# Performance work log

Hardware: AMD Instinct MI355X
Metric: run time of the kernel (lower is better)

Reference implementation:

```python
import jax, jax.numpy as jnp
import numpy as np

NUM_LAYERS = 3  # min_num_layers == max_num_layers == 3 (deterministic stochastic depth)
LN_EPS = 1e-5


def setup_inputs() -> dict:
    key = jax.random.key(0)
    k1, k2, k3 = jax.random.split(key, 3)
    N, d, F = 8, 16, 512  # (batch, in_dim=out_dim, num_features)
    x = jax.random.normal(k1, (N, d, F), dtype=jnp.float32)
    W = jax.random.normal(k2, (d, F, F, d), dtype=jnp.float32)  # recurrent weight
    A = jax.random.uniform(k3, (2, F, F), dtype=jnp.float32)    # transition mats, steps 1..2
    return {"x": x, "W": W, "A": A}


def _contract(h, W, a):
    # h: (N,d,F), W: (d,F,F,o), a: (F,F) -> (N,o,F)
    # Equivalent to (h.unsqueeze(-1).unsqueeze(-1) * (W * a[...,None])).sum(1).sum(1).transpose(1,2)
    return jnp.einsum('ndf,dfgo,fg->nog', h, W, a)


def _layer_norm(y):
    # torch applies layer_norm over the channel dim (axis 1 of (N,o,F)), no affine params
    m = y.mean(axis=1, keepdims=True)
    v = y.var(axis=1, keepdims=True)
    return (y - m) / jnp.sqrt(v + LN_EPS)


def reference(x, W, A):
    history = [x]
    for i in range(1, NUM_LAYERS):
        # recurrent + residual branch: average contributions from all previous layers
        ys = [_contract(history[j], W, A[i - j - 1]) for j in range(i)]
        y = jnp.mean(jnp.stack(ys, axis=0), axis=0)
        y = _layer_norm(y)
        history.append(y)
    return history[-1]  # return_layers='last'
```

## Files before the change

### kernel.cpp

```cpp
#include <hip/hip_runtime.h>
#include <stdint.h>


#define F_CHUNK 32
#define N_CHUNKS 16

__global__ void k0_prep_x(const float* __restrict__ x, float* __restrict__ xT) {
    int idx = blockIdx.x * blockDim.x + threadIdx.x;
    int n = idx & 7, d = (idx >> 3) & 15, f = idx >> 7;
    xT[idx] = x[n * 8192 + d * 512 + f];
}

template <bool PASS_A>
__global__ __launch_bounds__(256)
void k_contract(const float* __restrict__ W, const float* __restrict__ A,
                const float* __restrict__ xT,
                float* __restrict__ p0, float* __restrict__ p1) {
    const int t  = threadIdx.x;
    const int fc = blockIdx.x;
    const int ct = blockIdx.y;
    const int g  = ct * 16 + (t >> 4);
    const int o  = t & 15;
    const int col = g * 16 + o;
    const int f0 = fc * F_CHUNK;

    float c0[8], c1[8];
#pragma unroll
    for (int n = 0; n < 8; ++n) { c0[n] = 0.f; c1[n] = 0.f; }

    const float* Wc = W + col;
    for (int f = f0; f < f0 + F_CHUNK; ++f) {
        float w[16];
#pragma unroll
        for (int d = 0; d < 16; ++d)
            w[d] = Wc[(size_t)d * 4194304 + (size_t)f * 8192];

        const float* xf = xT + f * 128;
        float p[8];
#pragma unroll
        for (int n = 0; n < 8; ++n) p[n] = 0.f;
#pragma unroll
        for (int d = 0; d < 16; ++d) {
#pragma unroll
            for (int n = 0; n < 8; ++n)
                p[n] = fmaf(xf[d * 8 + n], w[d], p[n]);
        }

        float a0 = A[f * 512 + g];
#pragma unroll
        for (int n = 0; n < 8; ++n) c0[n] = fmaf(a0, p[n], c0[n]);
        if constexpr (PASS_A) {
            float a1 = A[262144 + f * 512 + g];
#pragma unroll
            for (int n = 0; n < 8; ++n) c1[n] = fmaf(a1, p[n], c1[n]);
        }
    }

    size_t base = (((size_t)fc * 512 + g) * 16 + o) * 8;
#pragma unroll
    for (int n = 0; n < 8; ++n) p0[base + n] = c0[n];
    if constexpr (PASS_A) {
#pragma unroll
        for (int n = 0; n < 8; ++n) p1[base + n] = c1[n];
    }
}

__global__ __launch_bounds__(128)
void k_reduce_ln(const float* __restrict__ part, float* __restrict__ outT) {
    __shared__ float sh[16][8];
    int g = blockIdx.x;
    int t = threadIdx.x;
    int o = t >> 3, n = t & 7;
    float s = 0.f;
    for (int ch = 0; ch < 16; ++ch)
        s += part[(((size_t)ch * 512 + g) * 16 + o) * 8 + n];
    sh[o][n] = s;
    __syncthreads();
    float m = 0.f, v = 0.f;
#pragma unroll
    for (int oo = 0; oo < 16; ++oo) { float y = sh[oo][n]; m += y; v += y * y; }
    m *= (1.f / 16.f);
    v = v * (1.f / 16.f) - m * m;
    float r = rsqrtf(v + 1e-5f);
    outT[((size_t)g * 16 + o) * 8 + n] = (s - m) * r;
}

__global__ __launch_bounds__(128)
void k_final(const float* __restrict__ p1, const float* __restrict__ p2,
             float* __restrict__ out) {
    __shared__ float sh[16][8];
    int g = blockIdx.x;
    int t = threadIdx.x;
    int o = t >> 3, n = t & 7;
    float s = 0.f;
    for (int ch = 0; ch < 16; ++ch) {
        size_t idx = (((size_t)ch * 512 + g) * 16 + o) * 8 + n;
        s += p1[idx] + p2[idx];
    }
    s *= 0.5f;
    sh[o][n] = s;
    __syncthreads();
    float m = 0.f, v = 0.f;
#pragma unroll
    for (int oo = 0; oo < 16; ++oo) { float y = sh[oo][n]; m += y; v += y * y; }
    m *= (1.f / 16.f);
    v = v * (1.f / 16.f) - m * m;
    float r = rsqrtf(v + 1e-5f);
    out[n * 8192 + o * 512 + g] = (s - m) * r;
}

extern "C" void kernel_launch(void* const* d_in, const int* in_sizes, int n_in,
                              void* d_out, int out_size, void* d_ws, size_t ws_size,
                              hipStream_t stream) {
    const float* x = (const float*)d_in[0];
    const float* W = (const float*)d_in[1];
    const float* A = (const float*)d_in[2];
    float* out = (float*)d_out;

    float* ws  = (float*)d_ws;
    float* xT  = ws;
    float* xT2 = ws + 65536;
    float* c0p = ws + 131072;
    float* c1p = c0p + 1048576;
    float* c2p = c1p + 1048576;

    k0_prep_x<<<256, 256, 0, stream>>>(x, xT);
    k_contract<true ><<<dim3(N_CHUNKS, 32), 256, 0, stream>>>(W, A, xT,  c0p, c1p);
    k_reduce_ln<<<512, 128, 0, stream>>>(c0p, xT2);
    k_contract<false><<<dim3(N_CHUNKS, 32), 256, 0, stream>>>(W, A, xT2, c2p, nullptr);
    k_final<<<512, 128, 0, stream>>>(c1p, c2p, out);
}
```

Measured before the change: 417.3 us.

## Split F finer, vectorize W loads to float2, reverse second pass order

```diff
diff --git a/kernel.cpp b/kernel.cpp
--- a/kernel.cpp
+++ b/kernel.cpp
@@ -2,8 +2,8 @@
 #include <stdint.h>
 
 
-#define F_CHUNK 32
-#define N_CHUNKS 16
+#define FC  8
+#define NCH 64
 
 __global__ void k0_prep_x(const float* __restrict__ x, float* __restrict__ xT) {
     int idx = blockIdx.x * blockDim.x + threadIdx.x;
@@ -12,56 +12,72 @@
 }
 
 template <bool PASS_A>
-__global__ __launch_bounds__(256)
+__global__ __launch_bounds__(256, 4)
 void k_contract(const float* __restrict__ W, const float* __restrict__ A,
                 const float* __restrict__ xT,
                 float* __restrict__ p0, float* __restrict__ p1) {
-    const int t  = threadIdx.x;
-    const int fc = blockIdx.x;
-    const int ct = blockIdx.y;
-    const int g  = ct * 16 + (t >> 4);
-    const int o  = t & 15;
-    const int col = g * 16 + o;
-    const int f0 = fc * F_CHUNK;
+    const int t   = threadIdx.x;
+    const int fc  = blockIdx.x;
+    const int ct  = blockIdx.y;
+    const int col = ct * 512 + t * 2;
+    const int g   = col >> 4;
+    const int f0  = fc * FC;
 
-    float c0[8], c1[8];
+    float c0x[8], c0y[8], c1x[8], c1y[8];
 #pragma unroll
-    for (int n = 0; n < 8; ++n) { c0[n] = 0.f; c1[n] = 0.f; }
+    for (int n = 0; n < 8; ++n) { c0x[n] = 0.f; c0y[n] = 0.f; c1x[n] = 0.f; c1y[n] = 0.f; }
 
     const float* Wc = W + col;
-    for (int f = f0; f < f0 + F_CHUNK; ++f) {
-        float w[16];
+#pragma unroll
+    for (int ff = 0; ff < FC; ++ff) {
+        const int f = PASS_A ? (f0 + ff) : (f0 + FC - 1 - ff);
+
+        float2 w[16];
 #pragma unroll
         for (int d = 0; d < 16; ++d)
-            w[d] = Wc[(size_t)d * 4194304 + (size_t)f * 8192];
+            w[d] = *reinterpret_cast<const float2*>(Wc + (size_t)d * 4194304 + (size_t)f * 8192);
 
         const float* xf = xT + f * 128;
-        float p[8];
+        float px[8], py[8];
 #pragma unroll
-        for (int n = 0; n < 8; ++n) p[n] = 0.f;
+        for (int n = 0; n < 8; ++n) { px[n] = 0.f; py[n] = 0.f; }
 #pragma unroll
         for (int d = 0; d < 16; ++d) {
 #pragma unroll
-            for (int n = 0; n < 8; ++n)
-                p[n] = fmaf(xf[d * 8 + n], w[d], p[n]);
+            for (int n = 0; n < 8; ++n) {
+                float xv = xf[d * 8 + n];
+                px[n] = fmaf(xv, w[d].x, px[n]);
+                py[n] = fmaf(xv, w[d].y, py[n]);
+            }
         }
 
         float a0 = A[f * 512 + g];
 #pragma unroll
-        for (int n = 0; n < 8; ++n) c0[n] = fmaf(a0, p[n], c0[n]);
+        for (int n = 0; n < 8; ++n) {
+            c0x[n] = fmaf(a0, px[n], c0x[n]);
+            c0y[n] = fmaf(a0, py[n], c0y[n]);
+        }
         if constexpr (PASS_A) {
             float a1 = A[262144 + f * 512 + g];
 #pragma unroll
-            for (int n = 0; n < 8; ++n) c1[n] = fmaf(a1, p[n], c1[n]);
+            for (int n = 0; n < 8; ++n) {
+                c1x[n] = fmaf(a1, px[n], c1x[n]);
+                c1y[n] = fmaf(a1, py[n], c1y[n]);
+            }
         }
     }
 
-    size_t base = (((size_t)fc * 512 + g) * 16 + o) * 8;
-#pragma unroll
-    for (int n = 0; n < 8; ++n) p0[base + n] = c0[n];
+    float4* dst0 = reinterpret_cast<float4*>(p0 + ((size_t)fc * 8192 + col) * 8);
+    dst0[0] = make_float4(c0x[0], c0x[1], c0x[2], c0x[3]);
+    dst0[1] = make_float4(c0x[4], c0x[5], c0x[6], c0x[7]);
+    dst0[2] = make_float4(c0y[0], c0y[1], c0y[2], c0y[3]);
+    dst0[3] = make_float4(c0y[4], c0y[5], c0y[6], c0y[7]);
     if constexpr (PASS_A) {
-#pragma unroll
-        for (int n = 0; n < 8; ++n) p1[base + n] = c1[n];
+        float4* dst1 = reinterpret_cast<float4*>(p1 + ((size_t)fc * 8192 + col) * 8);
+        dst1[0] = make_float4(c1x[0], c1x[1], c1x[2], c1x[3]);
+        dst1[1] = make_float4(c1x[4], c1x[5], c1x[6], c1x[7]);
+        dst1[2] = make_float4(c1y[0], c1y[1], c1y[2], c1y[3]);
+        dst1[3] = make_float4(c1y[4], c1y[5], c1y[6], c1y[7]);
     }
 }
 
@@ -71,9 +87,16 @@
     int g = blockIdx.x;
     int t = threadIdx.x;
     int o = t >> 3, n = t & 7;
-    float s = 0.f;
-    for (int ch = 0; ch < 16; ++ch)
-        s += part[(((size_t)ch * 512 + g) * 16 + o) * 8 + n];
+    size_t base = ((size_t)g * 16 + o) * 8 + n;
+    float s0 = 0.f, s1 = 0.f, s2 = 0.f, s3 = 0.f;
+#pragma unroll
+    for (int ch = 0; ch < NCH; ch += 4) {
+        s0 += part[(size_t)(ch + 0) * 65536 + base];
+        s1 += part[(size_t)(ch + 1) * 65536 + base];
+        s2 += part[(size_t)(ch + 2) * 65536 + base];
+        s3 += part[(size_t)(ch + 3) * 65536 + base];
+    }
+    float s = (s0 + s1) + (s2 + s3);
     sh[o][n] = s;
     __syncthreads();
     float m = 0.f, v = 0.f;
@@ -82,7 +105,7 @@
     m *= (1.f / 16.f);
     v = v * (1.f / 16.f) - m * m;
     float r = rsqrtf(v + 1e-5f);
-    outT[((size_t)g * 16 + o) * 8 + n] = (s - m) * r;
+    outT[base] = (s - m) * r;
 }
 
 __global__ __launch_bounds__(128)
@@ -92,12 +115,16 @@
     int g = blockIdx.x;
     int t = threadIdx.x;
     int o = t >> 3, n = t & 7;
-    float s = 0.f;
-    for (int ch = 0; ch < 16; ++ch) {
-        size_t idx = (((size_t)ch * 512 + g) * 16 + o) * 8 + n;
-        s += p1[idx] + p2[idx];
+    size_t base = ((size_t)g * 16 + o) * 8 + n;
+    float s0 = 0.f, s1 = 0.f, s2 = 0.f, s3 = 0.f;
+#pragma unroll
+    for (int ch = 0; ch < NCH; ch += 2) {
+        size_t i0 = (size_t)(ch + 0) * 65536 + base;
+        size_t i1 = (size_t)(ch + 1) * 65536 + base;
+        s0 += p1[i0]; s1 += p2[i0];
+        s2 += p1[i1]; s3 += p2[i1];
     }
-    s *= 0.5f;
+    float s = 0.5f * ((s0 + s1) + (s2 + s3));
     sh[o][n] = s;
     __syncthreads();
     float m = 0.f, v = 0.f;
@@ -121,12 +148,12 @@
     float* xT  = ws;
     float* xT2 = ws + 65536;
     float* c0p = ws + 131072;
-    float* c1p = c0p + 1048576;
-    float* c2p = c1p + 1048576;
+    float* c1p = c0p + 4194304;
+    float* c2p = c1p + 4194304;
 
     k0_prep_x<<<256, 256, 0, stream>>>(x, xT);
-    k_contract<true ><<<dim3(N_CHUNKS, 32), 256, 0, stream>>>(W, A, xT,  c0p, c1p);
+    k_contract<true ><<<dim3(NCH, 16), 256, 0, stream>>>(W, A, xT,  c0p, c1p);
     k_reduce_ln<<<512, 128, 0, stream>>>(c0p, xT2);
-    k_contract<false><<<dim3(N_CHUNKS, 32), 256, 0, stream>>>(W, A, xT2, c2p, nullptr);
+    k_contract<false><<<dim3(NCH, 16), 256, 0, stream>>>(W, A, xT2, c2p, nullptr);
     k_final<<<512, 128, 0, stream>>>(c1p, c2p, out);
 }
```

Measured after the change: 582.6 us. 39.6% more time.

## Fuse x transpose and reduce+layernorm into contract kernels via shared memory staging

Applied to the files above, without the earlier changes.

```diff
diff --git a/kernel.cpp b/kernel.cpp
--- a/kernel.cpp
+++ b/kernel.cpp
@@ -2,87 +2,118 @@
 #include <stdint.h>
 
 
-#define F_CHUNK 32
-#define N_CHUNKS 16
+#define FC   32
+#define NCH  16
 
-__global__ void k0_prep_x(const float* __restrict__ x, float* __restrict__ xT) {
-    int idx = blockIdx.x * blockDim.x + threadIdx.x;
-    int n = idx & 7, d = (idx >> 3) & 15, f = idx >> 7;
-    xT[idx] = x[n * 8192 + d * 512 + f];
-}
-
-template <bool PASS_A>
+template <bool SECOND>
 __global__ __launch_bounds__(256)
 void k_contract(const float* __restrict__ W, const float* __restrict__ A,
-                const float* __restrict__ xT,
+                const float* __restrict__ in,
                 float* __restrict__ p0, float* __restrict__ p1) {
+    __shared__ float sx[FC][16][8];
+    __shared__ float sA0[FC][16];
+    __shared__ float sA1[FC][16];
+
     const int t  = threadIdx.x;
     const int fc = blockIdx.x;
     const int ct = blockIdx.y;
-    const int g  = ct * 16 + (t >> 4);
-    const int o  = t & 15;
-    const int col = g * 16 + o;
-    const int f0 = fc * F_CHUNK;
+    const int f0 = fc * FC;
+
+    if constexpr (!SECOND) {
+#pragma unroll
+        for (int k = 0; k < 16; ++k) {
+            int idx = k * 256 + t;
+            int fl = idx >> 7, d = (idx >> 3) & 15, n = idx & 7;
+            sx[fl][d][n] = in[n * 8192 + d * 512 + f0 + fl];
+        }
+    } else {
+#pragma unroll
+        for (int k = 0; k < 16; ++k) {
+            int idx = k * 256 + t;
+            int fl = idx >> 7, o = (idx >> 3) & 15, n = idx & 7;
+            float s = 0.f;
+#pragma unroll
+            for (int ch = 0; ch < NCH; ++ch)
+                s += in[(((size_t)ch * 512 + f0 + fl) * 16 + o) * 8 + n];
+            sx[fl][o][n] = s;
+        }
+        __syncthreads();
+        {
+            int fl = t >> 3, n = t & 7;
+            float m = 0.f, v = 0.f;
+#pragma unroll
+            for (int oo = 0; oo < 16; ++oo) { float y = sx[fl][oo][n]; m += y; v += y * y; }
+            m *= (1.f / 16.f);
+            v = v * (1.f / 16.f) - m * m;
+            float r = rsqrtf(v + 1e-5f);
+#pragma unroll
+            for (int oo = 0; oo < 16; ++oo) sx[fl][oo][n] = (sx[fl][oo][n] - m) * r;
+        }
+    }
+    {
+#pragma unroll
+        for (int k = 0; k < 2; ++k) {
+            int idx = k * 256 + t;
+            int fl = idx >> 4, gl = idx & 15;
+            sA0[fl][gl] = A[(size_t)(f0 + fl) * 512 + ct * 16 + gl];
+            if constexpr (!SECOND)
+                sA1[fl][gl] = A[262144 + (size_t)(f0 + fl) * 512 + ct * 16 + gl];
+        }
+    }
+    __syncthreads();
+
+    const int gl  = t >> 4;
+    const int o   = t & 15;
+    const int col = (ct * 16 + gl) * 16 + o;
+    const float* Wc = W + col;
 
     float c0[8], c1[8];
 #pragma unroll
     for (int n = 0; n < 8; ++n) { c0[n] = 0.f; c1[n] = 0.f; }
 
-    const float* Wc = W + col;
-    for (int f = f0; f < f0 + F_CHUNK; ++f) {
+    for (int fl = 0; fl < FC; ++fl) {
+        const int f = f0 + fl;
         float w[16];
 #pragma unroll
         for (int d = 0; d < 16; ++d)
             w[d] = Wc[(size_t)d * 4194304 + (size_t)f * 8192];
 
-        const float* xf = xT + f * 128;
         float p[8];
 #pragma unroll
         for (int n = 0; n < 8; ++n) p[n] = 0.f;
 #pragma unroll
         for (int d = 0; d < 16; ++d) {
-#pragma unroll
-            for (int n = 0; n < 8; ++n)
-                p[n] = fmaf(xf[d * 8 + n], w[d], p[n]);
+            float4 xa = *reinterpret_cast<const float4*>(&sx[fl][d][0]);
+            float4 xb = *reinterpret_cast<const float4*>(&sx[fl][d][4]);
+            p[0] = fmaf(xa.x, w[d], p[0]);
+            p[1] = fmaf(xa.y, w[d], p[1]);
+            p[2] = fmaf(xa.z, w[d], p[2]);
+            p[3] = fmaf(xa.w, w[d], p[3]);
+            p[4] = fmaf(xb.x, w[d], p[4]);
+            p[5] = fmaf(xb.y, w[d], p[5]);
+            p[6] = fmaf(xb.z, w[d], p[6]);
+            p[7] = fmaf(xb.w, w[d], p[7]);
         }
 
-        float a0 = A[f * 512 + g];
+        const float a0 = sA0[fl][gl];
 #pragma unroll
         for (int n = 0; n < 8; ++n) c0[n] = fmaf(a0, p[n], c0[n]);
-        if constexpr (PASS_A) {
-            float a1 = A[262144 + f * 512 + g];
+        if constexpr (!SECOND) {
+            const float a1 = sA1[fl][gl];
 #pragma unroll
             for (int n = 0; n < 8; ++n) c1[n] = fmaf(a1, p[n], c1[n]);
         }
     }
 
-    size_t base = (((size_t)fc * 512 + g) * 16 + o) * 8;
-#pragma unroll
-    for (int n = 0; n < 8; ++n) p0[base + n] = c0[n];
-    if constexpr (PASS_A) {
-#pragma unroll
-        for (int n = 0; n < 8; ++n) p1[base + n] = c1[n];
+    size_t base = ((size_t)fc * 8192 + col) * 8;
+    float4* dst0 = reinterpret_cast<float4*>(p0 + base);
+    dst0[0] = make_float4(c0[0], c0[1], c0[2], c0[3]);
+    dst0[1] = make_float4(c0[4], c0[5], c0[6], c0[7]);
+    if constexpr (!SECOND) {
+        float4* dst1 = reinterpret_cast<float4*>(p1 + base);
+        dst1[0] = make_float4(c1[0], c1[1], c1[2], c1[3]);
+        dst1[1] = make_float4(c1[4], c1[5], c1[6], c1[7]);
     }
-}
-
-__global__ __launch_bounds__(128)
-void k_reduce_ln(const float* __restrict__ part, float* __restrict__ outT) {
-    __shared__ float sh[16][8];
-    int g = blockIdx.x;
-    int t = threadIdx.x;
-    int o = t >> 3, n = t & 7;
-    float s = 0.f;
-    for (int ch = 0; ch < 16; ++ch)
-        s += part[(((size_t)ch * 512 + g) * 16 + o) * 8 + n];
-    sh[o][n] = s;
-    __syncthreads();
-    float m = 0.f, v = 0.f;
-#pragma unroll
-    for (int oo = 0; oo < 16; ++oo) { float y = sh[oo][n]; m += y; v += y * y; }
-    m *= (1.f / 16.f);
-    v = v * (1.f / 16.f) - m * m;
-    float r = rsqrtf(v + 1e-5f);
-    outT[((size_t)g * 16 + o) * 8 + n] = (s - m) * r;
 }
 
 __global__ __launch_bounds__(128)
@@ -92,12 +123,14 @@
     int g = blockIdx.x;
     int t = threadIdx.x;
     int o = t >> 3, n = t & 7;
-    float s = 0.f;
-    for (int ch = 0; ch < 16; ++ch) {
+    float s0 = 0.f, s1 = 0.f;
+#pragma unroll
+    for (int ch = 0; ch < NCH; ++ch) {
         size_t idx = (((size_t)ch * 512 + g) * 16 + o) * 8 + n;
-        s += p1[idx] + p2[idx];
+        s0 += p1[idx];
+        s1 += p2[idx];
     }
-    s *= 0.5f;
+    float s = 0.5f * (s0 + s1);
     sh[o][n] = s;
     __syncthreads();
     float m = 0.f, v = 0.f;
@@ -118,15 +151,11 @@
     float* out = (float*)d_out;
 
     float* ws  = (float*)d_ws;
-    float* xT  = ws;
-    float* xT2 = ws + 65536;
-    float* c0p = ws + 131072;
+    float* c0p = ws;
     float* c1p = c0p + 1048576;
     float* c2p = c1p + 1048576;
 
-    k0_prep_x<<<256, 256, 0, stream>>>(x, xT);
-    k_contract<true ><<<dim3(N_CHUNKS, 32), 256, 0, stream>>>(W, A, xT,  c0p, c1p);
-    k_reduce_ln<<<512, 128, 0, stream>>>(c0p, xT2);
-    k_contract<false><<<dim3(N_CHUNKS, 32), 256, 0, stream>>>(W, A, xT2, c2p, nullptr);
+    k_contract<false><<<dim3(NCH, 32), 256, 0, stream>>>(W, A, x,   c0p, c1p);
+    k_contract<true ><<<dim3(NCH, 32), 256, 0, stream>>>(W, A, c0p, c2p, nullptr);
     k_final<<<512, 128, 0, stream>>>(c1p, c2p, out);
 }
```

Result: no change. 412.9 us (-1.1%).
